# Kernel optimization log

Measured on AMD Instinct MI355X. Metric: run time of the kernel, lower is better.

The kernel has to match this reference:

```python
import jax, jax.numpy as jnp
import numpy as np

NEG_INF = -9e15  # matches the torch -9000000000000000.0 mask value
LRELU_SLOPE = 0.01  # torch nn.LeakyReLU default


def setup_inputs() -> dict:
    key = jax.random.key(0)
    k1, k2, k3, k4 = jax.random.split(key, 4)
    N, F_in, F_out = 8192, 256, 128
    x = jax.random.normal(k1, (N, F_in), dtype=jnp.float32)
    adj = jax.random.randint(k2, (N, N), 0, 2, dtype=jnp.int32)
    # xavier_uniform with gain=1.414
    limW = 1.414 * np.sqrt(6.0 / (F_in + F_out))
    W = jax.random.uniform(k3, (F_in, F_out), minval=-limW, maxval=limW, dtype=jnp.float32)
    lima = 1.414 * np.sqrt(6.0 / (2 * F_out + 1))
    a = jax.random.uniform(k4, (2 * F_out, 1), minval=-lima, maxval=lima, dtype=jnp.float32)
    return {"x": x, "adj": adj, "W": W, "a": a}


def reference(x, adj, W, a):
    # h: [N, F_out]
    h = x @ W
    F_out = h.shape[1]
    a1 = a[:F_out, 0]   # attention vector for source node i
    a2 = a[F_out:, 0]   # attention vector for target node j
    # e[i, j] = leaky_relu(h_i . a1 + h_j . a2) -- equivalent to the repeat/cat
    # construction without materializing the [N, N, 2F] tensor.
    e = (h @ a1)[:, None] + (h @ a2)[None, :]  # [N, N]
    e = jnp.where(e > 0, e, LRELU_SLOPE * e)
    scores = jnp.where(adj > 0, e, NEG_INF)
    attention = jax.nn.softmax(scores, axis=1)  # dropout omitted (eval mode)
    h_prime = attention @ h  # [N, F_out]
    return jax.nn.elu(h_prime)
```

## Files before the change

### kernel.cpp

```cpp
#include <hip/hip_runtime.h>
#include <hip/hip_bf16.h>
#include <stdint.h>


#define N_NODES 8192
#define F_INF   256
#define F_OUT   128
#define LRELU   0.01f

typedef __bf16 bf16x8 __attribute__((ext_vector_type(8)));
typedef float  f32x4  __attribute__((ext_vector_type(4)));
using bf16 = __hip_bfloat16;

__device__ __forceinline__ float b2f(bf16 v) { return __bfloat162float(v); }
__device__ __forceinline__ bf16  f2b(float v) { return __float2bfloat16(v); }

__global__ __launch_bounds__(256) void k_xw(const float* __restrict__ x,
                                            const float* __restrict__ W,
                                            const float* __restrict__ a,
                                            bf16* __restrict__ hT,
                                            float* __restrict__ s1,
                                            float* __restrict__ s2) {
    __shared__ __align__(16) bf16 WTh[F_OUT][F_INF + 8];
    __shared__ __align__(16) bf16 WTl[F_OUT][F_INF + 8];
    __shared__ __align__(16) bf16 XSh[32][72];
    __shared__ __align__(16) bf16 XSl[32][72];
    __shared__ float a1s[F_OUT], a2s[F_OUT], s1L[32], s2L[32];
    const int tid  = threadIdx.x;
    const int lane = tid & 63, wave = tid >> 6;
    const int i0   = blockIdx.x * 32;
    if (tid < F_OUT) { a1s[tid] = a[tid]; a2s[tid] = a[tid + F_OUT]; }
    if (tid < 32)    { s1L[tid] = 0.f; s2L[tid] = 0.f; }
    for (int idx = tid; idx < (F_INF * F_OUT) / 8; idx += 256) {
        int k  = idx >> 4;
        int n0 = (idx & 15) * 8;
        const float* src = W + (size_t)k * F_OUT + n0;
        float4 va = *(const float4*)(src);
        float4 vb = *(const float4*)(src + 4);
        float v[8] = {va.x, va.y, va.z, va.w, vb.x, vb.y, vb.z, vb.w};
#pragma unroll
        for (int c = 0; c < 8; ++c) {
            bf16 hi = f2b(v[c]);
            WTh[n0 + c][k] = hi;
            WTl[n0 + c][k] = f2b(v[c] - b2f(hi));
        }
    }
    __syncthreads();
    f32x4 acc[4];
#pragma unroll
    for (int t = 0; t < 4; ++t) acc[t] = {0.f, 0.f, 0.f, 0.f};
    const int m = lane & 15, quad = lane >> 4;
    const int rt = wave & 1, cH = wave >> 1;
    for (int kc = 0; kc < F_INF / 64; ++kc) {
        const int k0 = kc * 64;
        {
            int part = tid & 7;
            int r    = tid >> 3;
            const float* src = x + (size_t)(i0 + r) * F_INF + k0 + part * 8;
            float4 va = *(const float4*)(src);
            float4 vb = *(const float4*)(src + 4);
            float v[8] = {va.x, va.y, va.z, va.w, vb.x, vb.y, vb.z, vb.w};
            __align__(16) bf16 th[8];
            __align__(16) bf16 tl[8];
#pragma unroll
            for (int c = 0; c < 8; ++c) {
                bf16 hi = f2b(v[c]);
                th[c] = hi;
                tl[c] = f2b(v[c] - b2f(hi));
            }
            *(uint4*)(&XSh[r][part * 8]) = *(const uint4*)th;
            *(uint4*)(&XSl[r][part * 8]) = *(const uint4*)tl;
        }
        __syncthreads();
#pragma unroll
        for (int ks = 0; ks < 2; ++ks) {
            bf16x8 ah = *(const bf16x8*)(&XSh[rt * 16 + m][ks * 32 + quad * 8]);
            bf16x8 al = *(const bf16x8*)(&XSl[rt * 16 + m][ks * 32 + quad * 8]);
#pragma unroll
            for (int c = 0; c < 4; ++c) {
                const int ct = cH * 4 + c;
                bf16x8 bh = *(const bf16x8*)(&WTh[ct * 16 + m][k0 + ks * 32 + quad * 8]);
                bf16x8 bl = *(const bf16x8*)(&WTl[ct * 16 + m][k0 + ks * 32 + quad * 8]);
                acc[c] = __builtin_amdgcn_mfma_f32_16x16x32_bf16(al, bh, acc[c], 0, 0, 0);
                acc[c] = __builtin_amdgcn_mfma_f32_16x16x32_bf16(ah, bl, acc[c], 0, 0, 0);
                acc[c] = __builtin_amdgcn_mfma_f32_16x16x32_bf16(ah, bh, acc[c], 0, 0, 0);
            }
        }
        __syncthreads();
    }
    float p1[4] = {0.f, 0.f, 0.f, 0.f}, p2[4] = {0.f, 0.f, 0.f, 0.f};
#pragma unroll
    for (int c = 0; c < 4; ++c) {
        const int f = (cH * 4 + c) * 16 + m;
        const float w1 = a1s[f], w2 = a2s[f];
#pragma unroll
        for (int r = 0; r < 4; ++r) { p1[r] += acc[c][r] * w1; p2[r] += acc[c][r] * w2; }
    }
#pragma unroll
    for (int r = 0; r < 4; ++r) {
        const int row = rt * 16 + quad * 4 + r;
        atomicAdd(&s1L[row], p1[r]);
        atomicAdd(&s2L[row], p2[r]);
    }
#pragma unroll
    for (int c = 0; c < 4; ++c) {
        const int f = (cH * 4 + c) * 16 + m;
#pragma unroll
        for (int r = 0; r < 4; ++r) {
            const int i = i0 + rt * 16 + quad * 4 + r;
            hT[(size_t)f * N_NODES + i] = f2b(acc[c][r]);
        }
    }
    __syncthreads();
    if (tid < 32) { s1[i0 + tid] = s1L[tid]; s2[i0 + tid] = s2L[tid]; }
}

__global__ __launch_bounds__(256) void k_max(const float* __restrict__ s2,
                                             float* __restrict__ mg) {
    __shared__ float red[256];
    int tid = threadIdx.x;
    float m = -1e30f;
    for (int j = tid; j < N_NODES; j += 256) m = fmaxf(m, s2[j]);
    red[tid] = m;
    __syncthreads();
    for (int s = 128; s > 0; s >>= 1) {
        if (tid < s) red[tid] = fmaxf(red[tid], red[tid + s]);
        __syncthreads();
    }
    if (tid == 0) mg[0] = red[0];
}

__global__ __launch_bounds__(256, 4) void k_attn(const int* __restrict__ adj,
                                                 const float* __restrict__ s1g,
                                                 const float* __restrict__ s2g,
                                                 const float* __restrict__ mg,
                                                 const bf16* __restrict__ hT,
                                                 float* __restrict__ Of,
                                                 float* __restrict__ lp) {
    __shared__ __align__(16) bf16 HS[F_OUT][72];
    __shared__ float s2s[2048];
    __shared__ float lsum[32];
    const int tid  = threadIdx.x;
    const int lane = tid & 63, wave = tid >> 6;
    const int m = lane & 15, quad = lane >> 4;
    const int rt = wave & 1, kh = wave >> 1;
    const int i0    = blockIdx.x * 32;
    const int jq    = blockIdx.y;
    const int jbase = jq * 2048;
    const int irow  = i0 + rt * 16 + m;
    const float s1v = s1g[irow];
    const float tmi = s1v + mg[0];
    const float mi  = fmaxf(tmi, LRELU * tmi);
    if (tid < 32) lsum[tid] = 0.f;
    for (int c = tid; c < 2048 / 4; c += 256)
        *(float4*)&s2s[c * 4] = *(const float4*)(s2g + jbase + c * 4);
    const int part = tid & 7, fr = tid >> 3;
    const bf16* hTp = hT + jbase + part * 8;
    {
        uint4 v0 = *(const uint4*)(hTp + (size_t)(fr +  0) * N_NODES);
        uint4 v1 = *(const uint4*)(hTp + (size_t)(fr + 32) * N_NODES);
        uint4 v2 = *(const uint4*)(hTp + (size_t)(fr + 64) * N_NODES);
        uint4 v3 = *(const uint4*)(hTp + (size_t)(fr + 96) * N_NODES);
        *(uint4*)&HS[fr +  0][part * 8] = v0;
        *(uint4*)&HS[fr + 32][part * 8] = v1;
        *(uint4*)&HS[fr + 64][part * 8] = v2;
        *(uint4*)&HS[fr + 96][part * 8] = v3;
    }
    const int jloc = kh * 32 + quad * 8;
    const int4* arowp = (const int4*)(adj + (size_t)irow * N_NODES + jbase);
    int4 av0 = arowp[0 * 16 + jloc / 4];
    int4 av1 = arowp[0 * 16 + jloc / 4 + 1];
    float lacc = 0.f;
    f32x4 acc[8];
#pragma unroll
    for (int c = 0; c < 8; ++c) acc[c] = {0.f, 0.f, 0.f, 0.f};
    __syncthreads();

    for (int jc = 0; jc < 32; ++jc) {
        const int jn = (jc < 31) ? jc + 1 : 31;
        uint4 h0 = *(const uint4*)(hTp + (size_t)(fr +  0) * N_NODES + jn * 64);
        uint4 h1 = *(const uint4*)(hTp + (size_t)(fr + 32) * N_NODES + jn * 64);
        uint4 h2 = *(const uint4*)(hTp + (size_t)(fr + 64) * N_NODES + jn * 64);
        uint4 h3 = *(const uint4*)(hTp + (size_t)(fr + 96) * N_NODES + jn * 64);
        const int am[8] = {av0.x, av0.y, av0.z, av0.w, av1.x, av1.y, av1.z, av1.w};
        const float* s2p = &s2s[jc * 64 + jloc];
        __align__(16) bf16 a8[8];
#pragma unroll
        for (int t = 0; t < 8; ++t) {
            float e = s1v + s2p[t];
            e = fmaxf(e, LRELU * e);
            float w = (am[t] > 0) ? __expf(e - mi) : 0.f;
            bf16 b = f2b(w);
            a8[t] = b;
            lacc += b2f(b);
        }
        bf16x8 afrag = *(const bf16x8*)a8;
        av0 = arowp[jn * 16 + jloc / 4];
        av1 = arowp[jn * 16 + jloc / 4 + 1];
#pragma unroll
        for (int c = 0; c < 8; ++c) {
            bf16x8 bfr = *(const bf16x8*)(&HS[c * 16 + m][jloc]);
            acc[c] = __builtin_amdgcn_mfma_f32_16x16x32_bf16(afrag, bfr, acc[c], 0, 0, 0);
        }
        __syncthreads();
        *(uint4*)&HS[fr +  0][part * 8] = h0;
        *(uint4*)&HS[fr + 32][part * 8] = h1;
        *(uint4*)&HS[fr + 64][part * 8] = h2;
        *(uint4*)&HS[fr + 96][part * 8] = h3;
        __syncthreads();
    }
    lacc += __shfl_xor(lacc, 16);
    lacc += __shfl_xor(lacc, 32);
    if (quad == 0) atomicAdd(&lsum[rt * 16 + m], lacc);
    __syncthreads();
    if (tid < 32) lp[(size_t)jq * N_NODES + i0 + tid] = lsum[tid];
    float* scr = (float*)&HS[0][0];
    if (kh == 1) {
#pragma unroll
        for (int c = 0; c < 8; ++c)
#pragma unroll
            for (int r = 0; r < 4; ++r)
                scr[(rt * 16 + quad * 4 + r) * 128 + c * 16 + m] = acc[c][r];
    }
    __syncthreads();
    if (kh == 0) {
#pragma unroll
        for (int c = 0; c < 8; ++c)
#pragma unroll
            for (int r = 0; r < 4; ++r) {
                const int row = rt * 16 + quad * 4 + r;
                const int f   = c * 16 + m;
                Of[((size_t)jq * N_NODES + i0 + row) * F_OUT + f] =
                    acc[c][r] + scr[row * 128 + f];
            }
    }
}

__global__ __launch_bounds__(256) void k_comb(const float* __restrict__ Of,
                                              const float* __restrict__ lp,
                                              float* __restrict__ out) {
    size_t gid = (size_t)blockIdx.x * 256 + threadIdx.x;
    int i = (int)(gid >> 7);
    float s = 0.f, l = 0.f;
#pragma unroll
    for (int q = 0; q < 4; ++q) {
        s += Of[(size_t)q * (N_NODES * (size_t)F_OUT) + gid];
        l += lp[q * N_NODES + i];
    }
    float o = s / l;
    out[gid] = o > 0.f ? o : __expf(o) - 1.f;
}

extern "C" void kernel_launch(void* const* d_in, const int* in_sizes, int n_in,
                              void* d_out, int out_size, void* d_ws, size_t ws_size,
                              hipStream_t stream) {
    (void)out_size; (void)ws_size;
    const float* x   = nullptr;
    const int*   adj = nullptr;
    const float* W   = nullptr;
    const float* a   = nullptr;
    for (int ii = 0; ii < n_in; ++ii) {
        int sz = in_sizes[ii];
        if      (sz == N_NODES * F_INF)  x   = (const float*)d_in[ii];
        else if (sz == F_INF * F_OUT)    W   = (const float*)d_in[ii];
        else if (sz == 2 * F_OUT)        a   = (const float*)d_in[ii];
        else                             adj = (const int*)d_in[ii];
    }
    float* out = (float*)d_out;

    char* ws = (char*)d_ws;
    bf16*  hT = (bf16*)ws;  ws += (size_t)F_OUT * N_NODES * 2;
    float* s1 = (float*)ws; ws += N_NODES * 4;
    float* s2 = (float*)ws; ws += N_NODES * 4;
    float* mg = (float*)ws; ws += 256;
    float* lp = (float*)ws; ws += 4 * N_NODES * 4;
    float* Of = (float*)ws;

    k_xw  <<<N_NODES / 32, 256, 0, stream>>>(x, W, a, hT, s1, s2);
    k_max <<<1, 256, 0, stream>>>(s2, mg);
    k_attn<<<dim3(N_NODES / 32, 4), 256, 0, stream>>>(adj, s1, s2, mg, hT, Of, lp);
    k_comb<<<(N_NODES * F_OUT) / 256, 256, 0, stream>>>(Of, lp, out);
}
```

Measured before the change: 437.5 us.

## Double-buffer H tiles via direct global-to-LDS loads and fuse max reduction

The single-block max kernel is removed: k_xw now writes per-block maxima of s2 and k_attn reduces those 256 partials itself. In k_attn the H tile is double-buffered in LDS and filled with global_load_lds through an XOR-swizzled layout, dropping one of the two barriers per step and the register staging. s2 values are read straight from global memory instead of an LDS copy, and MFMA priority is raised with s_setprio. This saves a launch and per-iteration synchronisation, but relies on the swizzle matching between the store and read sides and on async-load ordering at the barrier.

```diff
diff --git a/kernel.cpp b/kernel.cpp
--- a/kernel.cpp
+++ b/kernel.cpp
@@ -14,13 +14,20 @@
 
 __device__ __forceinline__ float b2f(bf16 v) { return __bfloat162float(v); }
 __device__ __forceinline__ bf16  f2b(float v) { return __float2bfloat16(v); }
+
+__device__ __forceinline__ void gll16(const void* g, void* l) {
+    __builtin_amdgcn_global_load_lds(
+        (const __attribute__((address_space(1))) uint32_t*)g,
+        (__attribute__((address_space(3))) uint32_t*)l, 16, 0, 0);
+}
 
 __global__ __launch_bounds__(256) void k_xw(const float* __restrict__ x,
                                             const float* __restrict__ W,
                                             const float* __restrict__ a,
                                             bf16* __restrict__ hT,
                                             float* __restrict__ s1,
-                                            float* __restrict__ s2) {
+                                            float* __restrict__ s2,
+                                            float* __restrict__ mgp) {
     __shared__ __align__(16) bf16 WTh[F_OUT][F_INF + 8];
     __shared__ __align__(16) bf16 WTl[F_OUT][F_INF + 8];
     __shared__ __align__(16) bf16 XSh[32][72];
@@ -112,33 +119,25 @@
         }
     }
     __syncthreads();
-    if (tid < 32) { s1[i0 + tid] = s1L[tid]; s2[i0 + tid] = s2L[tid]; }
-}
-
-__global__ __launch_bounds__(256) void k_max(const float* __restrict__ s2,
-                                             float* __restrict__ mg) {
-    __shared__ float red[256];
-    int tid = threadIdx.x;
-    float m = -1e30f;
-    for (int j = tid; j < N_NODES; j += 256) m = fmaxf(m, s2[j]);
-    red[tid] = m;
-    __syncthreads();
-    for (int s = 128; s > 0; s >>= 1) {
-        if (tid < s) red[tid] = fmaxf(red[tid], red[tid + s]);
-        __syncthreads();
-    }
-    if (tid == 0) mg[0] = red[0];
+    if (tid < 32) {
+        s1[i0 + tid] = s1L[tid];
+        s2[i0 + tid] = s2L[tid];
+        float m2 = s2L[tid];
+#pragma unroll
+        for (int s = 16; s > 0; s >>= 1) m2 = fmaxf(m2, __shfl_xor(m2, s));
+        if (tid == 0) mgp[blockIdx.x] = m2;
+    }
 }
 
 __global__ __launch_bounds__(256, 4) void k_attn(const int* __restrict__ adj,
                                                  const float* __restrict__ s1g,
                                                  const float* __restrict__ s2g,
-                                                 const float* __restrict__ mg,
+                                                 const float* __restrict__ mgp,
                                                  const bf16* __restrict__ hT,
                                                  float* __restrict__ Of,
                                                  float* __restrict__ lp) {
-    __shared__ __align__(16) bf16 HS[F_OUT][72];
-    __shared__ float s2s[2048];
+    __shared__ __align__(16) bf16 HS2[2][F_OUT][64];
+    __shared__ float wred[4];
     __shared__ float lsum[32];
     const int tid  = threadIdx.x;
     const int lane = tid & 63, wave = tid >> 6;
@@ -149,45 +148,49 @@
     const int jbase = jq * 2048;
     const int irow  = i0 + rt * 16 + m;
     const float s1v = s1g[irow];
-    const float tmi = s1v + mg[0];
-    const float mi  = fmaxf(tmi, LRELU * tmi);
+    float mv = mgp[tid];
+#pragma unroll
+    for (int s = 32; s > 0; s >>= 1) mv = fmaxf(mv, __shfl_xor(mv, s));
+    if (lane == 0) wred[wave] = mv;
     if (tid < 32) lsum[tid] = 0.f;
-    for (int c = tid; c < 2048 / 4; c += 256)
-        *(float4*)&s2s[c * 4] = *(const float4*)(s2g + jbase + c * 4);
     const int part = tid & 7, fr = tid >> 3;
-    const bf16* hTp = hT + jbase + part * 8;
-    {
-        uint4 v0 = *(const uint4*)(hTp + (size_t)(fr +  0) * N_NODES);
-        uint4 v1 = *(const uint4*)(hTp + (size_t)(fr + 32) * N_NODES);
-        uint4 v2 = *(const uint4*)(hTp + (size_t)(fr + 64) * N_NODES);
-        uint4 v3 = *(const uint4*)(hTp + (size_t)(fr + 96) * N_NODES);
-        *(uint4*)&HS[fr +  0][part * 8] = v0;
-        *(uint4*)&HS[fr + 32][part * 8] = v1;
-        *(uint4*)&HS[fr + 64][part * 8] = v2;
-        *(uint4*)&HS[fr + 96][part * 8] = v3;
-    }
+    const int psw  = (part ^ (fr & 7)) * 8;
+    const bf16* hTp = hT + jbase + psw;
+#pragma unroll
+    for (int g = 0; g < 4; ++g)
+        gll16(hTp + (size_t)(fr + g * 32) * N_NODES, &HS2[0][fr + g * 32][part * 8]);
     const int jloc = kh * 32 + quad * 8;
-    const int4* arowp = (const int4*)(adj + (size_t)irow * N_NODES + jbase);
-    int4 av0 = arowp[0 * 16 + jloc / 4];
-    int4 av1 = arowp[0 * 16 + jloc / 4 + 1];
+    const int4*   arowp = (const int4*)(adj + (size_t)irow * N_NODES + jbase);
+    const float4* srowp = (const float4*)(s2g + jbase);
+    int4   avA = arowp[jloc / 4],     avB = arowp[jloc / 4 + 1];
+    float4 svA = srowp[jloc / 4],     svB = srowp[jloc / 4 + 1];
     float lacc = 0.f;
     f32x4 acc[8];
 #pragma unroll
     for (int c = 0; c < 8; ++c) acc[c] = {0.f, 0.f, 0.f, 0.f};
     __syncthreads();
+    const float mgv = fmaxf(fmaxf(wred[0], wred[1]), fmaxf(wred[2], wred[3]));
+    const float tmi = s1v + mgv;
+    const float mi  = fmaxf(tmi, LRELU * tmi);
+    const int slotsw = ((kh * 4 + quad) ^ (m & 7)) * 8;
 
     for (int jc = 0; jc < 32; ++jc) {
+        const int cur = jc & 1;
+        if (jc < 31) {
+#pragma unroll
+            for (int g = 0; g < 4; ++g)
+                gll16(hTp + (size_t)(fr + g * 32) * N_NODES + (jc + 1) * 64,
+                      &HS2[cur ^ 1][fr + g * 32][part * 8]);
+        }
         const int jn = (jc < 31) ? jc + 1 : 31;
-        uint4 h0 = *(const uint4*)(hTp + (size_t)(fr +  0) * N_NODES + jn * 64);
-        uint4 h1 = *(const uint4*)(hTp + (size_t)(fr + 32) * N_NODES + jn * 64);
-        uint4 h2 = *(const uint4*)(hTp + (size_t)(fr + 64) * N_NODES + jn * 64);
-        uint4 h3 = *(const uint4*)(hTp + (size_t)(fr + 96) * N_NODES + jn * 64);
-        const int am[8] = {av0.x, av0.y, av0.z, av0.w, av1.x, av1.y, av1.z, av1.w};
-        const float* s2p = &s2s[jc * 64 + jloc];
+        int4   navA = arowp[jn * 16 + jloc / 4], navB = arowp[jn * 16 + jloc / 4 + 1];
+        float4 nsvA = srowp[jn * 16 + jloc / 4], nsvB = srowp[jn * 16 + jloc / 4 + 1];
+        const int   am[8] = {avA.x, avA.y, avA.z, avA.w, avB.x, avB.y, avB.z, avB.w};
+        const float sm[8] = {svA.x, svA.y, svA.z, svA.w, svB.x, svB.y, svB.z, svB.w};
         __align__(16) bf16 a8[8];
 #pragma unroll
         for (int t = 0; t < 8; ++t) {
-            float e = s1v + s2p[t];
+            float e = s1v + sm[t];
             e = fmaxf(e, LRELU * e);
             float w = (am[t] > 0) ? __expf(e - mi) : 0.f;
             bf16 b = f2b(w);
@@ -195,18 +198,14 @@
             lacc += b2f(b);
         }
         bf16x8 afrag = *(const bf16x8*)a8;
-        av0 = arowp[jn * 16 + jloc / 4];
-        av1 = arowp[jn * 16 + jloc / 4 + 1];
+        __builtin_amdgcn_s_setprio(1);
 #pragma unroll
         for (int c = 0; c < 8; ++c) {
-            bf16x8 bfr = *(const bf16x8*)(&HS[c * 16 + m][jloc]);
+            bf16x8 bfr = *(const bf16x8*)(&HS2[cur][c * 16 + m][slotsw]);
             acc[c] = __builtin_amdgcn_mfma_f32_16x16x32_bf16(afrag, bfr, acc[c], 0, 0, 0);
         }
-        __syncthreads();
-        *(uint4*)&HS[fr +  0][part * 8] = h0;
-        *(uint4*)&HS[fr + 32][part * 8] = h1;
-        *(uint4*)&HS[fr + 64][part * 8] = h2;
-        *(uint4*)&HS[fr + 96][part * 8] = h3;
+        __builtin_amdgcn_s_setprio(0);
+        avA = navA; avB = navB; svA = nsvA; svB = nsvB;
         __syncthreads();
     }
     lacc += __shfl_xor(lacc, 16);
@@ -214,7 +213,7 @@
     if (quad == 0) atomicAdd(&lsum[rt * 16 + m], lacc);
     __syncthreads();
     if (tid < 32) lp[(size_t)jq * N_NODES + i0 + tid] = lsum[tid];
-    float* scr = (float*)&HS[0][0];
+    float* scr = (float*)&HS2[0][0][0];
     if (kh == 1) {
 #pragma unroll
         for (int c = 0; c < 8; ++c)
@@ -269,15 +268,14 @@
     float* out = (float*)d_out;
 
     char* ws = (char*)d_ws;
-    bf16*  hT = (bf16*)ws;  ws += (size_t)F_OUT * N_NODES * 2;
-    float* s1 = (float*)ws; ws += N_NODES * 4;
-    float* s2 = (float*)ws; ws += N_NODES * 4;
-    float* mg = (float*)ws; ws += 256;
-    float* lp = (float*)ws; ws += 4 * N_NODES * 4;
-    float* Of = (float*)ws;
-
-    k_xw  <<<N_NODES / 32, 256, 0, stream>>>(x, W, a, hT, s1, s2);
-    k_max <<<1, 256, 0, stream>>>(s2, mg);
-    k_attn<<<dim3(N_NODES / 32, 4), 256, 0, stream>>>(adj, s1, s2, mg, hT, Of, lp);
+    bf16*  hT  = (bf16*)ws;  ws += (size_t)F_OUT * N_NODES * 2;
+    float* s1  = (float*)ws; ws += N_NODES * 4;
+    float* s2  = (float*)ws; ws += N_NODES * 4;
+    float* mgp = (float*)ws; ws += 256 * 4;
+    float* lp  = (float*)ws; ws += 4 * N_NODES * 4;
+    float* Of  = (float*)ws;
+
+    k_xw  <<<N_NODES / 32, 256, 0, stream>>>(x, W, a, hT, s1, s2, mgp);
+    k_attn<<<dim3(N_NODES / 32, 4), 256, 0, stream>>>(adj, s1, s2, mgp, hT, Of, lp);
     k_comb<<<(N_NODES * F_OUT) / 256, 256, 0, stream>>>(Of, lp, out);
 }
```

New measurement: 437.2 us. About the same (-0.1%).
